# Optimization experiments

Hardware: AMD Instinct MI355X
Metric: run time of the kernel (lower is better)

Reference implementation:

```python
import jax, jax.numpy as jnp
import numpy as np
import math

B, NV, L = 64, 21, 2048
PATCH, STRIDE = 16, 8
PNUM = (L - PATCH) // STRIDE + 1  # 255 patches
D, H, NDIM = 128, 256, 2
PRED = 96
EPS = 1e-5
SCALE = 1.0 / math.sqrt(NDIM)  # MultiHeadEMA scale = sqrt(1/ndim)
# patch gather indices: [PNUM, PATCH]
PIDX = np.arange(PNUM)[:, None] * STRIDE + np.arange(PATCH)[None, :]


def setup_inputs() -> dict:
    key = jax.random.key(0)
    ks = jax.random.split(key, 24)
    nrm = lambda k, shape, std: std * jax.random.normal(k, shape, jnp.float32)
    inp = {}
    inp['x'] = jax.random.normal(ks[0], (B, NV, L), jnp.float32)
    # LEMencoder feature_projection: LEMblock(PATCH -> H -> D)
    inp['fp_w1'] = nrm(ks[1], (PATCH, H), 0.1)
    inp['fp_b1'] = jnp.zeros((H,), jnp.float32)
    inp['fp_w2'] = nrm(ks[2], (H, D), 0.1)
    inp['fp_b2'] = jnp.zeros((D,), jnp.float32)
    inp['fp_wr'] = nrm(ks[3], (PATCH, D), 0.1)
    inp['fp_br'] = jnp.zeros((D,), jnp.float32)
    inp['fp_g'] = jnp.ones((D,), jnp.float32)
    inp['fp_be'] = jnp.zeros((D,), jnp.float32)
    # 2 stacked encoder LEMblocks (D -> D -> D), leading layer axis
    inp['enc_w1'] = nrm(ks[4], (2, D, D), 0.05)
    inp['enc_b1'] = jnp.zeros((2, D), jnp.float32)
    inp['enc_w2'] = nrm(ks[5], (2, D, D), 0.05)
    inp['enc_b2'] = jnp.zeros((2, D), jnp.float32)
    inp['enc_wr'] = nrm(ks[6], (2, D, D), 0.05)
    inp['enc_br'] = jnp.zeros((2, D), jnp.float32)
    inp['enc_g'] = jnp.ones((2, D), jnp.float32)
    inp['enc_be'] = jnp.zeros((2, D), jnp.float32)
    # MultiHeadEMA params (unidirectional: kernel_dim == D)
    inp['ema_delta'] = nrm(ks[7], (D, NDIM, 1), 0.2)
    inp['ema_alpha'] = nrm(ks[8], (D, NDIM, 1), 0.2)
    val = jnp.array([1.0, -1.0], jnp.float32).reshape(1, NDIM, 1)  # +1/-1 alternating init
    inp['ema_beta'] = nrm(ks[9], (D, NDIM, 1), 0.02) + val
    inp['ema_gamma'] = nrm(ks[10], (D, NDIM), 1.0)
    inp['ema_omega'] = nrm(ks[11], (D,), 1.0)
    # Flatten_Head (shared): Linear(D*PNUM -> PRED)
    inp['head_w'] = nrm(ks[12], (D * PNUM, PRED), 0.02)
    inp['head_b'] = jnp.zeros((PRED,), jnp.float32)
    return inp


def _lemblock(x, w1, b1, w2, b2, wr, br, g, be):
    h = jax.nn.relu(x @ w1 + b1) @ w2 + b2
    y = h + (x @ wr + br)
    mu = jnp.mean(y, axis=-1, keepdims=True)
    var = jnp.mean(jnp.square(y - mu), axis=-1, keepdims=True)
    return g * (y - mu) * jax.lax.rsqrt(var + EPS) + be


def reference(x, fp_w1, fp_b1, fp_w2, fp_b2, fp_wr, fp_br, fp_g, fp_be,
              enc_w1, enc_b1, enc_w2, enc_b2, enc_wr, enc_br, enc_g, enc_be,
              ema_delta, ema_alpha, ema_beta, ema_gamma, ema_omega,
              head_w, head_b):
    # patching: [B, NV, L] -> [B*NV, PNUM, PATCH]
    z = x[:, :, PIDX].reshape(B * NV, PNUM, PATCH)
    # LEMencoder
    z = _lemblock(z, fp_w1, fp_b1, fp_w2, fp_b2, fp_wr, fp_br, fp_g, fp_be)
    for i in range(enc_w1.shape[0]):
        z = _lemblock(z, enc_w1[i], enc_b1[i], enc_w2[i], enc_b2[i],
                      enc_wr[i], enc_br[i], enc_g[i], enc_be[i])
    # MultiHeadEMA over patch (time) axis; input [Time=PNUM, Batch=B*NV, Channel=D]
    t = jnp.transpose(z, (1, 0, 2))
    residual = t * ema_omega
    xc = jnp.transpose(t, (1, 2, 0))  # [BN, D, PNUM]
    p = jax.nn.sigmoid(ema_delta)           # [D, N, 1]
    q = 1.0 - p * jax.nn.sigmoid(ema_alpha)  # [D, N, 1]
    vander = jnp.arange(PNUM, dtype=jnp.float32)[None, None, :] * jnp.log(q)  # [D, N, PNUM]
    kern = p * ema_beta * jnp.exp(vander)
    k = jnp.einsum('dnl,dn->dl', kern, ema_gamma * SCALE)  # [D, PNUM]
    n2 = 2 * PNUM
    out = jnp.fft.irfft(jnp.fft.rfft(xc, n=n2) * jnp.fft.rfft(k, n=n2), n=n2)[..., :PNUM]
    out = jax.nn.silu(jnp.transpose(out, (2, 0, 1)) + residual)  # [PNUM, BN, D]
    # Flatten_Head (shared): [B, NV, D, PNUM] -> flatten(-2) -> linear
    u = jnp.transpose(out, (1, 2, 0)).reshape(B, NV, D * PNUM)
    return u @ head_w + head_b  # [B, NV, PRED]
```

## Files before the change

kernel.cpp:

```cpp
#include <hip/hip_runtime.h>

typedef unsigned short u16;
typedef short bf8v __attribute__((ext_vector_type(8)));
typedef float f4v __attribute__((ext_vector_type(4)));
typedef float f16v __attribute__((ext_vector_type(16)));

#define DEV static __device__ __forceinline__

constexpr int BB   = 64;
constexpr int NV   = 21;
constexpr int BN   = BB * NV;
constexpr int PNUM = 255;
constexpr int D    = 128;
constexpr int PRED = 96;
constexpr int ROWS = BN * PNUM;
constexpr int KH   = D * PNUM;
constexpr int CH   = 30;
constexpr int KPC  = KH / CH;
constexpr int HITER = KPC / 32;
constexpr float EMA_SCALE = 0.70710678118654752440f;

DEV float bf2f(u16 h) { return __uint_as_float(((unsigned)h) << 16); }
DEV u16 f2bf(float f) {
  unsigned u = __float_as_uint(f);
  return (u16)((u + 0x7fffu + ((u >> 16) & 1u)) >> 16);
}
DEV unsigned pkbf2(float a, float b) {
  unsigned ua = __float_as_uint(a) + 0x8000u;
  unsigned ub = __float_as_uint(b) + 0x8000u;
  return __builtin_amdgcn_perm(ub, ua, 0x07060302u);
}
DEV bf8v mk4(unsigned a, unsigned b, unsigned c, unsigned d) {
  int4 t = {(int)a, (int)b, (int)c, (int)d};
  bf8v r;
  __builtin_memcpy(&r, &t, 16);
  return r;
}
DEV bf8v ld8(const u16* p) {
  bf8v r;
  __builtin_memcpy(&r, p, 16);
  return r;
}
DEV f4v mfma16(bf8v a, bf8v b, f4v c) {
  return __builtin_amdgcn_mfma_f32_16x16x32_bf16(a, b, c, 0, 0, 0);
}
DEV f16v mfma32(bf8v a, bf8v b, f16v c) {
  return __builtin_amdgcn_mfma_f32_32x32x16_bf16(a, b, c, 0, 0, 0);
}
DEV f16v zero16() {
  f16v r;
#pragma unroll
  for (int i = 0; i < 16; i++) r[i] = 0.f;
  return r;
}

#define FRAG_ASM(pk, ks, hh)                                                   \
  ({                                                                           \
    int _g = (ks) >> 1, _lw = 2 * ((ks) & 1);                                  \
    unsigned _A0 = pk[_g][_lw][0], _A1 = pk[_g][_lw][1];                       \
    unsigned _B0 = pk[_g][_lw + 1][0], _B1 = pk[_g][_lw + 1][1];               \
    unsigned _own0 = (hh) ? _B0 : _A0, _own1 = (hh) ? _B1 : _A1;               \
    unsigned _snd0 = (hh) ? _A0 : _B0, _snd1 = (hh) ? _A1 : _B1;               \
    unsigned _o0 = (unsigned)__shfl_xor((int)_snd0, 32, 64);                   \
    unsigned _o1 = (unsigned)__shfl_xor((int)_snd1, 32, 64);                   \
    mk4((hh) ? _o0 : _own0, (hh) ? _o1 : _own1,                                \
        (hh) ? _own0 : _o0, (hh) ? _own1 : _o1);                               \
  })

__global__ void swz_all(
    const float* __restrict__ fw1, const float* __restrict__ fw2,
    const float* __restrict__ fwr, const float* __restrict__ ew1,
    const float* __restrict__ ew2, const float* __restrict__ ewr,
    const float* __restrict__ hw, u16* __restrict__ wb, u16* __restrict__ wsh) {
  int b = blockIdx.x;
  if (b >= 560) {
    int i = (b - 560) * 256 + threadIdx.x;
    if (i >= KH * PRED) return;
    int kp = i / PRED, n = i - kp * PRED;
    int l = kp >> 7, d = kp & 127;
    wsh[((size_t)(kp >> 3) * PRED + n) * 8 + (kp & 7)] =
        f2bf(hw[(size_t)(d * PNUM + l) * PRED + n]);
    return;
  }
  const float* src; u16* dst; int K, N, Kp;
  if (b < 32)       { src = fw1; dst = wb;          K = 16;  N = 256; Kp = 32; }
  else if (b < 160) { b -= 32;  src = fw2; dst = wb + 8192;  K = 256; N = 128; Kp = 256; }
  else if (b < 176) { b -= 160; src = fwr; dst = wb + 40960; K = 16;  N = 128; Kp = 32; }
  else {
    int e = (b - 176) >> 6; b = (b - 176) & 63;
    int l = e / 3, w = e - 3 * l;
    const float* basep = (w == 0) ? ew1 : (w == 1) ? ew2 : ewr;
    src = basep + (size_t)l * 16384;
    dst = wb + 45056 + e * 16384;
    K = 128; N = 128; Kp = 128;
  }
  int i = b * 256 + threadIdx.x;
  if (i >= Kp * N) return;
  int k = i / N, n = i - k * N;
  u16 v = (k < K) ? f2bf(src[(size_t)k * N + n]) : (u16)0;
  dst[((size_t)(k >> 3) * N + n) * 8 + (k & 7)] = v;
}

__global__ __launch_bounds__(128, 2) void k_lem(
    const float* __restrict__ x,
    const u16* __restrict__ ws1, const float* __restrict__ b1,
    const u16* __restrict__ ws2, const u16* __restrict__ wsr,
    const float* __restrict__ b2, const float* __restrict__ br,
    const float* __restrict__ g, const float* __restrict__ be,
    const u16* __restrict__ wse, const float* __restrict__ eb1,
    const float* __restrict__ eb2, const float* __restrict__ ebr,
    const float* __restrict__ eg, const float* __restrict__ ebe,
    u16* __restrict__ zout) {
  __shared__ __align__(16) u16 zst[64 * 132];
  const int t = threadIdx.x;
  const int lane = t & 63, w = t >> 6;
  const int hh = lane >> 5, r5 = lane & 31;
  const int tile = blockIdx.x;
  const int row = tile * 64 + w * 32 + r5;

  bf8v azv;
  {
    unsigned R = (unsigned)row;
    unsigned bn = R / 255u;
    unsigned p = R - bn * 255u;
    const float* px = x + (size_t)bn * 2048u + p * 8u + hh * 8;
    float4 v0 = *(const float4*)px;
    float4 v1 = *(const float4*)(px + 4);
    azv = mk4(pkbf2(v0.x, v0.y), pkbf2(v0.z, v0.w),
              pkbf2(v1.x, v1.y), pkbf2(v1.z, v1.w));
  }

  unsigned hpk[8][4][2];
  unsigned zpk[4][4][2];

#pragma unroll
  for (int half = 0; half < 2; half++) {
    f16v a[4];
#pragma unroll
    for (int gg = 0; gg < 4; gg++) {
      bf8v wf = ld8(ws1 + ((size_t)(hh * 256 + (half * 4 + gg) * 32 + r5)) * 8);
      a[gg] = mfma32(wf, azv, zero16());
    }
#pragma unroll
    for (int gg = 0; gg < 4; gg++)
#pragma unroll
      for (int wq = 0; wq < 4; wq++) {
        int c0 = (half * 4 + gg) * 32 + wq * 8 + 4 * hh;
        float4 bv = *(const float4*)(b1 + c0);
        float v0 = fmaxf(a[gg][wq * 4 + 0] + bv.x, 0.f);
        float v1 = fmaxf(a[gg][wq * 4 + 1] + bv.y, 0.f);
        float v2 = fmaxf(a[gg][wq * 4 + 2] + bv.z, 0.f);
        float v3 = fmaxf(a[gg][wq * 4 + 3] + bv.w, 0.f);
        hpk[half * 4 + gg][wq][0] = pkbf2(v0, v1);
        hpk[half * 4 + gg][wq][1] = pkbf2(v2, v3);
      }
  }

  {
    f16v acc[4];
#pragma unroll
    for (int gg = 0; gg < 4; gg++) {
      bf8v wf = ld8(wsr + ((size_t)(hh * 128 + gg * 32 + r5)) * 8);
      acc[gg] = mfma32(wf, azv, zero16());
    }
    bf8v wq[2][4];
#pragma unroll
    for (int gg = 0; gg < 4; gg++)
      wq[0][gg] = ld8(ws2 + ((size_t)(hh * 128 + gg * 32 + r5)) * 8);
    bf8v bf_cur = FRAG_ASM(hpk, 0, hh);
#pragma unroll
    for (int ks = 0; ks < 16; ks++) {
      int cur = ks & 1;
      if (ks < 15) {
#pragma unroll
        for (int gg = 0; gg < 4; gg++)
          wq[cur ^ 1][gg] =
              ld8(ws2 + ((size_t)((2 * (ks + 1) + hh) * 128 + gg * 32 + r5)) * 8);
        bf8v bf_nxt = FRAG_ASM(hpk, ks + 1, hh);
#pragma unroll
        for (int gg = 0; gg < 4; gg++) acc[gg] = mfma32(wq[cur][gg], bf_cur, acc[gg]);
        bf_cur = bf_nxt;
      } else {
#pragma unroll
        for (int gg = 0; gg < 4; gg++) acc[gg] = mfma32(wq[cur][gg], bf_cur, acc[gg]);
      }
    }
    float s = 0.f, s2 = 0.f;
#pragma unroll
    for (int gg = 0; gg < 4; gg++)
#pragma unroll
      for (int wq4 = 0; wq4 < 4; wq4++) {
        int c0 = gg * 32 + wq4 * 8 + 4 * hh;
        float4 bv2 = *(const float4*)(b2 + c0);
        float4 bvr = *(const float4*)(br + c0);
        acc[gg][wq4 * 4 + 0] += bv2.x + bvr.x;
        acc[gg][wq4 * 4 + 1] += bv2.y + bvr.y;
        acc[gg][wq4 * 4 + 2] += bv2.z + bvr.z;
        acc[gg][wq4 * 4 + 3] += bv2.w + bvr.w;
#pragma unroll
        for (int sidx = 0; sidx < 4; sidx++) {
          float v = acc[gg][wq4 * 4 + sidx];
          s += v; s2 += v * v;
        }
      }
    s += __shfl_xor(s, 32, 64); s2 += __shfl_xor(s2, 32, 64);
    float mean = s * (1.f / 128.f);
    float rstd = rsqrtf(s2 * (1.f / 128.f) - mean * mean + 1e-5f);
#pragma unroll
    for (int gg = 0; gg < 4; gg++)
#pragma unroll
      for (int wq4 = 0; wq4 < 4; wq4++) {
        int c0 = gg * 32 + wq4 * 8 + 4 * hh;
        float4 gv = *(const float4*)(g + c0);
        float4 bv = *(const float4*)(be + c0);
        float v0 = (acc[gg][wq4 * 4 + 0] - mean) * rstd * gv.x + bv.x;
        float v1 = (acc[gg][wq4 * 4 + 1] - mean) * rstd * gv.y + bv.y;
        float v2 = (acc[gg][wq4 * 4 + 2] - mean) * rstd * gv.z + bv.z;
        float v3 = (acc[gg][wq4 * 4 + 3] - mean) * rstd * gv.w + bv.w;
        zpk[gg][wq4][0] = pkbf2(v0, v1);
        zpk[gg][wq4][1] = pkbf2(v2, v3);
      }
  }

#pragma unroll 1
  for (int L = 0; L < 2; L++) {
    const u16* w1p = wse + (size_t)(L * 3 + 0) * 16384;
    const u16* w2p = wse + (size_t)(L * 3 + 1) * 16384;
    const u16* wrp = wse + (size_t)(L * 3 + 2) * 16384;
    unsigned hp2[4][4][2];
    {
      f16v a2[4];
#pragma unroll
      for (int gg = 0; gg < 4; gg++) a2[gg] = zero16();
      bf8v wq[2][4];
#pragma unroll
      for (int gg = 0; gg < 4; gg++)
        wq[0][gg] = ld8(w1p + ((size_t)(hh * 128 + gg * 32 + r5)) * 8);
      bf8v bf_cur = FRAG_ASM(zpk, 0, hh);
#pragma unroll
      for (int ks = 0; ks < 8; ks++) {
        int cur = ks & 1;
        if (ks < 7) {
#pragma unroll
          for (int gg = 0; gg < 4; gg++)
            wq[cur ^ 1][gg] =
                ld8(w1p + ((size_t)((2 * (ks + 1) + hh) * 128 + gg * 32 + r5)) * 8);
          bf8v bf_nxt = FRAG_ASM(zpk, ks + 1, hh);
#pragma unroll
          for (int gg = 0; gg < 4; gg++) a2[gg] = mfma32(wq[cur][gg], bf_cur, a2[gg]);
          bf_cur = bf_nxt;
        } else {
#pragma unroll
          for (int gg = 0; gg < 4; gg++) a2[gg] = mfma32(wq[cur][gg], bf_cur, a2[gg]);
        }
      }
#pragma unroll
      for (int gg = 0; gg < 4; gg++)
#pragma unroll
        for (int wq4 = 0; wq4 < 4; wq4++) {
          int c0 = gg * 32 + wq4 * 8 + 4 * hh;
          float4 bv = *(const float4*)(eb1 + L * 128 + c0);
          float v0 = fmaxf(a2[gg][wq4 * 4 + 0] + bv.x, 0.f);
          float v1 = fmaxf(a2[gg][wq4 * 4 + 1] + bv.y, 0.f);
          float v2 = fmaxf(a2[gg][wq4 * 4 + 2] + bv.z, 0.f);
          float v3 = fmaxf(a2[gg][wq4 * 4 + 3] + bv.w, 0.f);
          hp2[gg][wq4][0] = pkbf2(v0, v1);
          hp2[gg][wq4][1] = pkbf2(v2, v3);
        }
    }
    f16v acc[4];
#pragma unroll
    for (int gg = 0; gg < 4; gg++) acc[gg] = zero16();
    {
      bf8v wq[2][4];
#pragma unroll
      for (int gg = 0; gg < 4; gg++)
        wq[0][gg] = ld8(w2p + ((size_t)(hh * 128 + gg * 32 + r5)) * 8);
      bf8v bf_cur = FRAG_ASM(hp2, 0, hh);
#pragma unroll
      for (int ks = 0; ks < 8; ks++) {
        int cur = ks & 1;
        if (ks < 7) {
#pragma unroll
          for (int gg = 0; gg < 4; gg++)
            wq[cur ^ 1][gg] =
                ld8(w2p + ((size_t)((2 * (ks + 1) + hh) * 128 + gg * 32 + r5)) * 8);
          bf8v bf_nxt = FRAG_ASM(hp2, ks + 1, hh);
#pragma unroll
          for (int gg = 0; gg < 4; gg++) acc[gg] = mfma32(wq[cur][gg], bf_cur, acc[gg]);
          bf_cur = bf_nxt;
        } else {
#pragma unroll
          for (int gg = 0; gg < 4; gg++) acc[gg] = mfma32(wq[cur][gg], bf_cur, acc[gg]);
        }
      }
#pragma unroll
      for (int gg = 0; gg < 4; gg++)
        wq[0][gg] = ld8(wrp + ((size_t)(hh * 128 + gg * 32 + r5)) * 8);
      bf_cur = FRAG_ASM(zpk, 0, hh);
#pragma unroll
      for (int ks = 0; ks < 8; ks++) {
        int cur = ks & 1;
        if (ks < 7) {
#pragma unroll
          for (int gg = 0; gg < 4; gg++)
            wq[cur ^ 1][gg] =
                ld8(wrp + ((size_t)((2 * (ks + 1) + hh) * 128 + gg * 32 + r5)) * 8);
          bf8v bf_nxt = FRAG_ASM(zpk, ks + 1, hh);
#pragma unroll
          for (int gg = 0; gg < 4; gg++) acc[gg] = mfma32(wq[cur][gg], bf_cur, acc[gg]);
          bf_cur = bf_nxt;
        } else {
#pragma unroll
          for (int gg = 0; gg < 4; gg++) acc[gg] = mfma32(wq[cur][gg], bf_cur, acc[gg]);
        }
      }
    }
    float s = 0.f, s2 = 0.f;
#pragma unroll
    for (int gg = 0; gg < 4; gg++)
#pragma unroll
      for (int wq4 = 0; wq4 < 4; wq4++) {
        int c0 = gg * 32 + wq4 * 8 + 4 * hh;
        float4 bv2 = *(const float4*)(eb2 + L * 128 + c0);
        float4 bvr = *(const float4*)(ebr + L * 128 + c0);
        acc[gg][wq4 * 4 + 0] += bv2.x + bvr.x;
        acc[gg][wq4 * 4 + 1] += bv2.y + bvr.y;
        acc[gg][wq4 * 4 + 2] += bv2.z + bvr.z;
        acc[gg][wq4 * 4 + 3] += bv2.w + bvr.w;
#pragma unroll
        for (int sidx = 0; sidx < 4; sidx++) {
          float v = acc[gg][wq4 * 4 + sidx];
          s += v; s2 += v * v;
        }
      }
    s += __shfl_xor(s, 32, 64); s2 += __shfl_xor(s2, 32, 64);
    float mean = s * (1.f / 128.f);
    float rstd = rsqrtf(s2 * (1.f / 128.f) - mean * mean + 1e-5f);
#pragma unroll
    for (int gg = 0; gg < 4; gg++)
#pragma unroll
      for (int wq4 = 0; wq4 < 4; wq4++) {
        int c0 = gg * 32 + wq4 * 8 + 4 * hh;
        float4 gv = *(const float4*)(eg + L * 128 + c0);
        float4 bv = *(const float4*)(ebe + L * 128 + c0);
        float v0 = (acc[gg][wq4 * 4 + 0] - mean) * rstd * gv.x + bv.x;
        float v1 = (acc[gg][wq4 * 4 + 1] - mean) * rstd * gv.y + bv.y;
        float v2 = (acc[gg][wq4 * 4 + 2] - mean) * rstd * gv.z + bv.z;
        float v3 = (acc[gg][wq4 * 4 + 3] - mean) * rstd * gv.w + bv.w;
        unsigned plo = pkbf2(v0, v1), phi = pkbf2(v2, v3);
        if (L == 0) {
          zpk[gg][wq4][0] = plo;
          zpk[gg][wq4][1] = phi;
        } else {
          uint2 pv = {plo, phi};
          *(uint2*)(zst + (w * 32 + r5) * 132 + c0) = pv;
        }
      }
  }

#pragma unroll
  for (int it = 0; it < 8; it++) {
    int lu = it * 64 + lane;
    int rr = lu >> 4, seg = lu & 15;
    int orow = w * 32 + rr;
    *(uint4*)(zout + ((size_t)tile * 64 + orow) * 128 + seg * 8) =
        *(const uint4*)(zst + orow * 132 + seg * 8);
  }
}

__global__ __launch_bounds__(128) void k_ema(
    u16* __restrict__ z,
    const float* __restrict__ pdel, const float* __restrict__ palp,
    const float* __restrict__ pbet, const float* __restrict__ pgam,
    const float* __restrict__ pome) {
  __shared__ __align__(16) u16 zc[64 * 128];
  const int t = threadIdx.x;
  const int bn = blockIdx.x;
  float p0 = 1.f / (1.f + __expf(-pdel[t * 2 + 0]));
  float p1 = 1.f / (1.f + __expf(-pdel[t * 2 + 1]));
  float q0 = 1.f - p0 / (1.f + __expf(-palp[t * 2 + 0]));
  float q1 = 1.f - p1 / (1.f + __expf(-palp[t * 2 + 1]));
  float w0 = p0 * pbet[t * 2 + 0] * pgam[t * 2 + 0] * EMA_SCALE;
  float w1 = p1 * pbet[t * 2 + 1] * pgam[t * 2 + 1] * EMA_SCALE;
  float om = pome[t];
  float s0 = 0.f, s1 = 0.f;
  u16* slab = z + (size_t)bn * KH;

  for (int ch = 0; ch < 4; ch++) {
    int nrow = (ch < 3) ? 64 : 63;
    int nval = nrow * 128;
    for (int i = t * 8; i < nval; i += 128 * 8)
      *(uint4*)(zc + i) = *(const uint4*)(slab + ch * 8192 + i);
    __syncthreads();
    for (int j0 = 0; j0 < nrow; j0 += 8) {
      float xs[8];
#pragma unroll
      for (int jj = 0; jj < 8; jj++)
        if (j0 + jj < nrow) xs[jj] = bf2f(zc[(j0 + jj) * 128 + t]);
#pragma unroll
      for (int jj = 0; jj < 8; jj++)
        if (j0 + jj < nrow) {
          float xv = xs[jj];
          s0 = q0 * s0 + xv;
          s1 = q1 * s1 + xv;
          float v = w0 * s0 + w1 * s1 + om * xv;
          xs[jj] = v / (1.f + __expf(-v));
        }
#pragma unroll
      for (int jj = 0; jj < 8; jj++)
        if (j0 + jj < nrow)
          zc[(j0 + jj) * 128 + t] = (u16)((__float_as_uint(xs[jj]) + 0x8000u) >> 16);
    }
    __syncthreads();
    for (int i = t * 8; i < nval; i += 128 * 8)
      *(uint4*)(slab + ch * 8192 + i) = *(const uint4*)(zc + i);
    __syncthreads();
  }
}

__global__ __launch_bounds__(256) void k_head(
    const u16* __restrict__ u, const u16* __restrict__ whs, float* __restrict__ part) {
  const int t = threadIdx.x;
  const int lane = t & 63, wid = t >> 6;
  const int quad = lane >> 4, lc = lane & 15;
  const int tile = blockIdx.x;
  const int ch = blockIdx.y;
  const int m0 = tile * 64 + wid * 16;
  const u16* Ab = u + (size_t)(m0 + lc) * KH + (size_t)ch * KPC;
  const int g0 = ch * (KPC / 8);
  f4v acc[6];
#pragma unroll
  for (int n = 0; n < 6; n++) acc[n] = (f4v){0.f, 0.f, 0.f, 0.f};
  bf8v a_nxt = ld8(Ab + quad * 8);
  bf8v b_nxt[6];
#pragma unroll
  for (int n = 0; n < 6; n++)
    b_nxt[n] = ld8(whs + ((size_t)(g0 + quad) * PRED + n * 16 + lc) * 8);
  for (int ks = 0; ks < HITER; ks++) {
    bf8v a_cur = a_nxt;
    bf8v b_cur[6];
#pragma unroll
    for (int n = 0; n < 6; n++) b_cur[n] = b_nxt[n];
    if (ks < HITER - 1) {
      a_nxt = ld8(Ab + (ks + 1) * 32 + quad * 8);
#pragma unroll
      for (int n = 0; n < 6; n++)
        b_nxt[n] = ld8(whs + ((size_t)(g0 + (ks + 1) * 4 + quad) * PRED + n * 16 + lc) * 8);
    }
#pragma unroll
    for (int n = 0; n < 6; n++) acc[n] = mfma16(a_cur, b_cur[n], acc[n]);
  }
#pragma unroll
  for (int n = 0; n < 6; n++) {
    int col = n * 16 + lc;
#pragma unroll
    for (int r = 0; r < 4; r++)
      part[((size_t)ch * BN + m0 + quad * 4 + r) * PRED + col] = acc[n][r];
  }
}

__global__ __launch_bounds__(256) void k_red(
    const float* __restrict__ part, const float* __restrict__ hb, float* __restrict__ out) {
  int i = blockIdx.x * 256 + threadIdx.x;
  if (i >= BN * PRED) return;
  int row = i / PRED, col = i - row * PRED;
  float s = hb[col];
#pragma unroll 5
  for (int c = 0; c < CH; c++) s += part[((size_t)c * BN + row) * PRED + col];
  out[i] = s;
}

extern "C" void kernel_launch(void* const* d_in, const int* in_sizes, int n_in,
                              void* d_out, int out_size, void* d_ws, size_t ws_size,
                              hipStream_t stream) {
  const float* x      = (const float*)d_in[0];
  const float* fp_w1  = (const float*)d_in[1];
  const float* fp_b1  = (const float*)d_in[2];
  const float* fp_w2  = (const float*)d_in[3];
  const float* fp_b2  = (const float*)d_in[4];
  const float* fp_wr  = (const float*)d_in[5];
  const float* fp_br  = (const float*)d_in[6];
  const float* fp_g   = (const float*)d_in[7];
  const float* fp_be  = (const float*)d_in[8];
  const float* enc_w1 = (const float*)d_in[9];
  const float* enc_b1 = (const float*)d_in[10];
  const float* enc_w2 = (const float*)d_in[11];
  const float* enc_b2 = (const float*)d_in[12];
  const float* enc_wr = (const float*)d_in[13];
  const float* enc_br = (const float*)d_in[14];
  const float* enc_g  = (const float*)d_in[15];
  const float* enc_be = (const float*)d_in[16];
  const float* e_del  = (const float*)d_in[17];
  const float* e_alp  = (const float*)d_in[18];
  const float* e_bet  = (const float*)d_in[19];
  const float* e_gam  = (const float*)d_in[20];
  const float* e_om   = (const float*)d_in[21];
  const float* head_w = (const float*)d_in[22];
  const float* head_b = (const float*)d_in[23];

  char* base = (char*)d_ws;
  u16* z3 = (u16*)base;
  const size_t EZB = (size_t)ROWS * 128 * 2;
  float* part = (float*)(base + EZB);
  const size_t PARTB = (size_t)CH * BN * PRED * 4;
  u16* wb = (u16*)(base + EZB + PARTB);
  u16* ws1 = wb;
  u16* ws2 = wb + 8192;
  u16* wsr = wb + 40960;
  u16* wse = wb + 45056;
  u16* wsh = wb + 143360;

  swz_all<<<560 + (KH * PRED + 255) / 256, 256, 0, stream>>>(
      fp_w1, fp_w2, fp_wr, enc_w1, enc_w2, enc_wr, head_w, wb, wsh);

  k_lem<<<ROWS / 64, 128, 0, stream>>>(x, ws1, fp_b1, ws2, wsr, fp_b2, fp_br, fp_g, fp_be,
                                       wse, enc_b1, enc_b2, enc_br, enc_g, enc_be, z3);
  k_ema<<<BN, 128, 0, stream>>>(z3, e_del, e_alp, e_bet, e_gam, e_om);
  k_head<<<dim3(21, CH), 256, 0, stream>>>(z3, wsh, part);
  k_red<<<(BN * PRED + 255) / 256, 256, 0, stream>>>(part, head_b, (float*)d_out);
}
```

Baseline: 390.3 us.

## Permute weight output columns to drop cross-lane shuffles; triple-buffer weight loads

The weight swizzle now permutes output columns (swapping bits 2 and 3 of n), so each MFMA accumulator lane already holds the K-fragment layout the next GEMM needs. This removes the __shfl_xor fragment assembly between chained GEMMs. Bias, gamma and beta indexing is remapped to match. Weight-fragment prefetch moves from double to triple buffering with distance two, and the two encoder W2/Wr loops are merged into one 16-step loop. The cost is more live registers for the extra buffer, which could hurt occupancy at two blocks per CU.

```diff
diff --git a/kernel.cpp b/kernel.cpp
--- a/kernel.cpp
+++ b/kernel.cpp
@@ -54,18 +54,9 @@
   return r;
 }
 
-#define FRAG_ASM(pk, ks, hh)                                                   \
-  ({                                                                           \
-    int _g = (ks) >> 1, _lw = 2 * ((ks) & 1);                                  \
-    unsigned _A0 = pk[_g][_lw][0], _A1 = pk[_g][_lw][1];                       \
-    unsigned _B0 = pk[_g][_lw + 1][0], _B1 = pk[_g][_lw + 1][1];               \
-    unsigned _own0 = (hh) ? _B0 : _A0, _own1 = (hh) ? _B1 : _A1;               \
-    unsigned _snd0 = (hh) ? _A0 : _B0, _snd1 = (hh) ? _A1 : _B1;               \
-    unsigned _o0 = (unsigned)__shfl_xor((int)_snd0, 32, 64);                   \
-    unsigned _o1 = (unsigned)__shfl_xor((int)_snd1, 32, 64);                   \
-    mk4((hh) ? _o0 : _own0, (hh) ? _o1 : _own1,                                \
-        (hh) ? _own0 : _o0, (hh) ? _own1 : _o1);                               \
-  })
+#define FRG(pk, ks)                                                            \
+  mk4(pk[(ks) >> 1][2 * ((ks) & 1)][0], pk[(ks) >> 1][2 * ((ks) & 1)][1],      \
+      pk[(ks) >> 1][2 * ((ks) & 1) + 1][0], pk[(ks) >> 1][2 * ((ks) & 1) + 1][1])
 
 __global__ void swz_all(
     const float* __restrict__ fw1, const float* __restrict__ fw2,
@@ -97,7 +88,8 @@
   int i = b * 256 + threadIdx.x;
   if (i >= Kp * N) return;
   int k = i / N, n = i - k * N;
-  u16 v = (k < K) ? f2bf(src[(size_t)k * N + n]) : (u16)0;
+  int np = (n & ~12) | ((n & 4) << 1) | ((n & 8) >> 1);
+  u16 v = (k < K) ? f2bf(src[(size_t)k * N + np]) : (u16)0;
   dst[((size_t)(k >> 3) * N + n) * 8 + (k & 7)] = v;
 }
 
@@ -145,7 +137,7 @@
     for (int gg = 0; gg < 4; gg++)
 #pragma unroll
       for (int wq = 0; wq < 4; wq++) {
-        int c0 = (half * 4 + gg) * 32 + wq * 8 + 4 * hh;
+        int c0 = (half * 4 + gg) * 32 + ((wq >> 1) << 4) + ((wq & 1) << 2) + (hh << 3);
         float4 bv = *(const float4*)(b1 + c0);
         float v0 = fmaxf(a[gg][wq * 4 + 0] + bv.x, 0.f);
         float v1 = fmaxf(a[gg][wq * 4 + 1] + bv.y, 0.f);
@@ -156,41 +148,40 @@
       }
   }
 
+  f16v acc[4];
   {
-    f16v acc[4];
-#pragma unroll
-    for (int gg = 0; gg < 4; gg++) {
-      bf8v wf = ld8(wsr + ((size_t)(hh * 128 + gg * 32 + r5)) * 8);
-      acc[gg] = mfma32(wf, azv, zero16());
-    }
-    bf8v wq[2][4];
+    bf8v wq[3][4];
+#pragma unroll
+    for (int b = 0; b < 2; b++)
+#pragma unroll
+      for (int gg = 0; gg < 4; gg++)
+        wq[b][gg] = ld8(ws2 + ((size_t)((2 * b + hh) * 128 + gg * 32 + r5)) * 8);
+    {
+      bf8v wr4[4];
+#pragma unroll
+      for (int gg = 0; gg < 4; gg++)
+        wr4[gg] = ld8(wsr + ((size_t)(hh * 128 + gg * 32 + r5)) * 8);
+#pragma unroll
+      for (int gg = 0; gg < 4; gg++) acc[gg] = mfma32(wr4[gg], azv, zero16());
+    }
+#pragma unroll
+    for (int u = 0; u < 16; u++) {
+      if (u + 2 < 16) {
+#pragma unroll
+        for (int gg = 0; gg < 4; gg++)
+          wq[(u + 2) % 3][gg] =
+              ld8(ws2 + ((size_t)((2 * (u + 2) + hh) * 128 + gg * 32 + r5)) * 8);
+      }
+      bf8v bfr = FRG(hpk, u);
+#pragma unroll
+      for (int gg = 0; gg < 4; gg++) acc[gg] = mfma32(wq[u % 3][gg], bfr, acc[gg]);
+    }
+    float s = 0.f, s2 = 0.f;
 #pragma unroll
     for (int gg = 0; gg < 4; gg++)
-      wq[0][gg] = ld8(ws2 + ((size_t)(hh * 128 + gg * 32 + r5)) * 8);
-    bf8v bf_cur = FRAG_ASM(hpk, 0, hh);
-#pragma unroll
-    for (int ks = 0; ks < 16; ks++) {
-      int cur = ks & 1;
-      if (ks < 15) {
-#pragma unroll
-        for (int gg = 0; gg < 4; gg++)
-          wq[cur ^ 1][gg] =
-              ld8(ws2 + ((size_t)((2 * (ks + 1) + hh) * 128 + gg * 32 + r5)) * 8);
-        bf8v bf_nxt = FRAG_ASM(hpk, ks + 1, hh);
-#pragma unroll
-        for (int gg = 0; gg < 4; gg++) acc[gg] = mfma32(wq[cur][gg], bf_cur, acc[gg]);
-        bf_cur = bf_nxt;
-      } else {
-#pragma unroll
-        for (int gg = 0; gg < 4; gg++) acc[gg] = mfma32(wq[cur][gg], bf_cur, acc[gg]);
-      }
-    }
-    float s = 0.f, s2 = 0.f;
-#pragma unroll
-    for (int gg = 0; gg < 4; gg++)
 #pragma unroll
       for (int wq4 = 0; wq4 < 4; wq4++) {
-        int c0 = gg * 32 + wq4 * 8 + 4 * hh;
+        int c0 = gg * 32 + ((wq4 >> 1) << 4) + ((wq4 & 1) << 2) + (hh << 3);
         float4 bv2 = *(const float4*)(b2 + c0);
         float4 bvr = *(const float4*)(br + c0);
         acc[gg][wq4 * 4 + 0] += bv2.x + bvr.x;
@@ -210,7 +201,7 @@
     for (int gg = 0; gg < 4; gg++)
 #pragma unroll
       for (int wq4 = 0; wq4 < 4; wq4++) {
-        int c0 = gg * 32 + wq4 * 8 + 4 * hh;
+        int c0 = gg * 32 + ((wq4 >> 1) << 4) + ((wq4 & 1) << 2) + (hh << 3);
         float4 gv = *(const float4*)(g + c0);
         float4 bv = *(const float4*)(be + c0);
         float v0 = (acc[gg][wq4 * 4 + 0] - mean) * rstd * gv.x + bv.x;
@@ -232,33 +223,29 @@
       f16v a2[4];
 #pragma unroll
       for (int gg = 0; gg < 4; gg++) a2[gg] = zero16();
-      bf8v wq[2][4];
+      bf8v wq[3][4];
+#pragma unroll
+      for (int b = 0; b < 2; b++)
+#pragma unroll
+        for (int gg = 0; gg < 4; gg++)
+          wq[b][gg] = ld8(w1p + ((size_t)((2 * b + hh) * 128 + gg * 32 + r5)) * 8);
+#pragma unroll
+      for (int u = 0; u < 8; u++) {
+        if (u + 2 < 8) {
+#pragma unroll
+          for (int gg = 0; gg < 4; gg++)
+            wq[(u + 2) % 3][gg] =
+                ld8(w1p + ((size_t)((2 * (u + 2) + hh) * 128 + gg * 32 + r5)) * 8);
+        }
+        bf8v bfr = FRG(zpk, u);
+#pragma unroll
+        for (int gg = 0; gg < 4; gg++) a2[gg] = mfma32(wq[u % 3][gg], bfr, a2[gg]);
+      }
 #pragma unroll
       for (int gg = 0; gg < 4; gg++)
-        wq[0][gg] = ld8(w1p + ((size_t)(hh * 128 + gg * 32 + r5)) * 8);
-      bf8v bf_cur = FRAG_ASM(zpk, 0, hh);
-#pragma unroll
-      for (int ks = 0; ks < 8; ks++) {
-        int cur = ks & 1;
-        if (ks < 7) {
-#pragma unroll
-          for (int gg = 0; gg < 4; gg++)
-            wq[cur ^ 1][gg] =
-                ld8(w1p + ((size_t)((2 * (ks + 1) + hh) * 128 + gg * 32 + r5)) * 8);
-          bf8v bf_nxt = FRAG_ASM(zpk, ks + 1, hh);
-#pragma unroll
-          for (int gg = 0; gg < 4; gg++) a2[gg] = mfma32(wq[cur][gg], bf_cur, a2[gg]);
-          bf_cur = bf_nxt;
-        } else {
-#pragma unroll
-          for (int gg = 0; gg < 4; gg++) a2[gg] = mfma32(wq[cur][gg], bf_cur, a2[gg]);
-        }
-      }
-#pragma unroll
-      for (int gg = 0; gg < 4; gg++)
 #pragma unroll
         for (int wq4 = 0; wq4 < 4; wq4++) {
-          int c0 = gg * 32 + wq4 * 8 + 4 * hh;
+          int c0 = gg * 32 + ((wq4 >> 1) << 4) + ((wq4 & 1) << 2) + (hh << 3);
           float4 bv = *(const float4*)(eb1 + L * 128 + c0);
           float v0 = fmaxf(a2[gg][wq4 * 4 + 0] + bv.x, 0.f);
           float v1 = fmaxf(a2[gg][wq4 * 4 + 1] + bv.y, 0.f);
@@ -268,52 +255,28 @@
           hp2[gg][wq4][1] = pkbf2(v2, v3);
         }
     }
-    f16v acc[4];
 #pragma unroll
     for (int gg = 0; gg < 4; gg++) acc[gg] = zero16();
     {
-      bf8v wq[2][4];
-#pragma unroll
-      for (int gg = 0; gg < 4; gg++)
-        wq[0][gg] = ld8(w2p + ((size_t)(hh * 128 + gg * 32 + r5)) * 8);
-      bf8v bf_cur = FRAG_ASM(hp2, 0, hh);
-#pragma unroll
-      for (int ks = 0; ks < 8; ks++) {
-        int cur = ks & 1;
-        if (ks < 7) {
+      bf8v wq[3][4];
+#pragma unroll
+      for (int b = 0; b < 2; b++)
+#pragma unroll
+        for (int gg = 0; gg < 4; gg++)
+          wq[b][gg] = ld8(w2p + ((size_t)((2 * b + hh) * 128 + gg * 32 + r5)) * 8);
+#pragma unroll
+      for (int u = 0; u < 16; u++) {
+        if (u + 2 < 16) {
+          int v = u + 2;
+          const u16* wp = (v < 8) ? w2p : wrp;
+          int kg = v & 7;
 #pragma unroll
           for (int gg = 0; gg < 4; gg++)
-            wq[cur ^ 1][gg] =
-                ld8(w2p + ((size_t)((2 * (ks + 1) + hh) * 128 + gg * 32 + r5)) * 8);
-          bf8v bf_nxt = FRAG_ASM(hp2, ks + 1, hh);
-#pragma unroll
-          for (int gg = 0; gg < 4; gg++) acc[gg] = mfma32(wq[cur][gg], bf_cur, acc[gg]);
-          bf_cur = bf_nxt;
-        } else {
-#pragma unroll
-          for (int gg = 0; gg < 4; gg++) acc[gg] = mfma32(wq[cur][gg], bf_cur, acc[gg]);
-        }
-      }
-#pragma unroll
-      for (int gg = 0; gg < 4; gg++)
-        wq[0][gg] = ld8(wrp + ((size_t)(hh * 128 + gg * 32 + r5)) * 8);
-      bf_cur = FRAG_ASM(zpk, 0, hh);
-#pragma unroll
-      for (int ks = 0; ks < 8; ks++) {
-        int cur = ks & 1;
-        if (ks < 7) {
-#pragma unroll
-          for (int gg = 0; gg < 4; gg++)
-            wq[cur ^ 1][gg] =
-                ld8(wrp + ((size_t)((2 * (ks + 1) + hh) * 128 + gg * 32 + r5)) * 8);
-          bf8v bf_nxt = FRAG_ASM(zpk, ks + 1, hh);
-#pragma unroll
-          for (int gg = 0; gg < 4; gg++) acc[gg] = mfma32(wq[cur][gg], bf_cur, acc[gg]);
-          bf_cur = bf_nxt;
-        } else {
-#pragma unroll
-          for (int gg = 0; gg < 4; gg++) acc[gg] = mfma32(wq[cur][gg], bf_cur, acc[gg]);
-        }
+            wq[v % 3][gg] = ld8(wp + ((size_t)((2 * kg + hh) * 128 + gg * 32 + r5)) * 8);
+        }
+        bf8v bfr = (u < 8) ? FRG(hp2, u) : FRG(zpk, (u - 8));
+#pragma unroll
+        for (int gg = 0; gg < 4; gg++) acc[gg] = mfma32(wq[u % 3][gg], bfr, acc[gg]);
       }
     }
     float s = 0.f, s2 = 0.f;
@@ -321,7 +284,7 @@
     for (int gg = 0; gg < 4; gg++)
 #pragma unroll
       for (int wq4 = 0; wq4 < 4; wq4++) {
-        int c0 = gg * 32 + wq4 * 8 + 4 * hh;
+        int c0 = gg * 32 + ((wq4 >> 1) << 4) + ((wq4 & 1) << 2) + (hh << 3);
         float4 bv2 = *(const float4*)(eb2 + L * 128 + c0);
         float4 bvr = *(const float4*)(ebr + L * 128 + c0);
         acc[gg][wq4 * 4 + 0] += bv2.x + bvr.x;
@@ -341,7 +304,7 @@
     for (int gg = 0; gg < 4; gg++)
 #pragma unroll
       for (int wq4 = 0; wq4 < 4; wq4++) {
-        int c0 = gg * 32 + wq4 * 8 + 4 * hh;
+        int c0 = gg * 32 + ((wq4 >> 1) << 4) + ((wq4 & 1) << 2) + (hh << 3);
         float4 gv = *(const float4*)(eg + L * 128 + c0);
         float4 bv = *(const float4*)(ebe + L * 128 + c0);
         float v0 = (acc[gg][wq4 * 4 + 0] - mean) * rstd * gv.x + bv.x;
```

Measured after the change: 408.6 us. 1.05x slower.
